# Kernel optimization log

Hardware: AMD Instinct MI355X
Metric: run time of the kernel (lower is better)

Reference implementation:

```python
import jax, jax.numpy as jnp
import numpy as np

BS = 131072
HID = 128

def _mlp(x, p):
    W1, b1, W2, b2, W3, b3 = p
    h = jnp.tanh(x @ W1 + b1)
    h = jnp.tanh(h @ W2 + b2)
    return h @ W3 + b3

def _inv2x2(M):
    # batched analytic 2x2 inverse, M: (bs,2,2)
    a, b = M[:, 0, 0], M[:, 0, 1]
    c, d = M[:, 1, 0], M[:, 1, 1]
    det = a * d - b * c
    row0 = jnp.stack([d, -b], axis=-1)
    row1 = jnp.stack([-c, a], axis=-1)
    return jnp.stack([row0, row1], axis=1) / det[:, None, None]

def _forward(y, hp, mp, gp):
    q3 = y[:, :3]           # (bs,3): x, cos q, sin q
    xq_dot = y[:, 3:5]      # (bs,2): x_dot, q_dot
    u = y[:, 5:6]           # (bs,1)
    cos_q = q3[:, 1:2]
    sin_q = q3[:, 2:3]

    def m_net(q):
        A = _mlp(q, mp).reshape(-1, 2, 2)
        return jnp.einsum('bij,bkj->bik', A, A) + jnp.eye(2, dtype=q.dtype)

    M_q_inv = m_net(q3)                                   # (bs,2,2) inverse mass matrix
    p = jnp.einsum('bij,bj->bi', _inv2x2(M_q_inv), xq_dot)  # momenta (bs,2)
    zp = jnp.concatenate([q3, p], axis=1)                 # (bs,5)

    # dH/d(x,cosq,sinq,p): samples are independent so grad of the batch-sum
    # gives per-sample gradients (matches torch.autograd.grad(H.sum(), ...)).
    dH = jax.grad(lambda z: _mlp(z, hp).sum())(zp)        # (bs,5)
    dHdx, dHdcos, dHdsin = dH[:, 0:1], dH[:, 1:2], dH[:, 2:3]
    dHdp = dH[:, 3:5]

    F = _mlp(q3, gp) * u                                  # u_dim == 1 branch
    dHdq = -sin_q * dHdcos + cos_q * dHdsin
    dx, dq = dHdp[:, 0:1], dHdp[:, 1:2]
    dp = jnp.concatenate([-dHdx, -dHdq], axis=1) + F      # (bs,2)

    # dM_inv/dt = (dM_inv/dq3) . dq3/dt  == JVP of m_net (replaces the 2x2
    # Python loop of per-element torch.autograd.grad calls).
    dq3dt = jnp.concatenate([dx, -sin_q * dq, cos_q * dq], axis=1)
    _, dM_inv_dt = jax.jvp(m_net, (q3,), (dq3dt,))        # (bs,2,2)

    ddq = jnp.einsum('bij,bj->bi', M_q_inv, dp) + jnp.einsum('bij,bj->bi', dM_inv_dt, p)
    return jnp.concatenate([dx, -sin_q * dq, cos_q * dq, ddq, jnp.zeros_like(u)], axis=1)

def setup_inputs():
    key = jax.random.key(0)
    ks = jax.random.split(key, 10)
    def w(k, fan_in, fan_out):
        return jax.random.normal(k, (fan_in, fan_out), dtype=jnp.float32) / np.float32(np.sqrt(fan_in))
    inp = {"t": 0, "y": jax.random.normal(ks[0], (BS, 6), dtype=jnp.float32)}
    dims = {"h": (5, 1), "m": (3, 4), "g": (3, 2)}
    i = 1
    for name, (din, dout) in dims.items():
        inp[name + "_W1"] = w(ks[i], din, HID)
        inp[name + "_b1"] = jnp.zeros((HID,), jnp.float32)
        inp[name + "_W2"] = w(ks[i + 1], HID, HID)
        inp[name + "_b2"] = jnp.zeros((HID,), jnp.float32)
        inp[name + "_W3"] = w(ks[i + 2], HID, dout)
        inp[name + "_b3"] = jnp.zeros((dout,), jnp.float32)
        i += 3
    return inp

def reference(t, y, h_W1, h_b1, h_W2, h_b2, h_W3, h_b3,
              m_W1, m_b1, m_W2, m_b2, m_W3, m_b3,
              g_W1, g_b1, g_W2, g_b2, g_W3, g_b3):
    hp = (h_W1, h_b1, h_W2, h_b2, h_W3, h_b3)
    mp = (m_W1, m_b1, m_W2, m_b2, m_W3, m_b3)
    gp = (g_W1, g_b1, g_W2, g_b2, g_W3, g_b3)
    return _forward(y, hp, mp, gp)
```

## Files before the change

kernel.cpp:

```cpp
#include <hip/hip_runtime.h>

#define T   32
#define LDX 132
#define NTH 512

enum { SF0 = 0, SF1, SO0, SO1, SO2, SO3, SM00, SM01, SM11, SP0, SP1,
       SV0, SV1, SV2, SDP0, SDP1, SM_N };

__device__ __forceinline__ float tanh_fast(float x) {
    float e = __expf(2.0f * x);
    return 1.0f - 2.0f / (e + 1.0f);
}

__device__ __forceinline__ float red16(float v) {
    v += __shfl_xor(v, 1);
    v += __shfl_xor(v, 2);
    v += __shfl_xor(v, 4);
    v += __shfl_xor(v, 8);
    return v;
}

template <class EPI>
__device__ __forceinline__ void mv128_fwd(const float* __restrict__ Wg,
                                          const float* in_row, int j0, EPI&& epi) {
    float acc[8];
#pragma unroll
    for (int jj = 0; jj < 8; ++jj) acc[jj] = 0.f;
    for (int i = 0; i < 128; i += 4) {
        float4 av = *(const float4*)(in_row + i);
#pragma unroll
        for (int s = 0; s < 4; ++s) {
            float a = (s == 0) ? av.x : (s == 1) ? av.y : (s == 2) ? av.z : av.w;
            const float4* wp = (const float4*)(Wg + (size_t)(i + s) * 128 + j0);
            float4 w0 = wp[0], w1 = wp[1];
            acc[0] += a * w0.x; acc[1] += a * w0.y; acc[2] += a * w0.z; acc[3] += a * w0.w;
            acc[4] += a * w1.x; acc[5] += a * w1.y; acc[6] += a * w1.z; acc[7] += a * w1.w;
        }
    }
#pragma unroll
    for (int jj = 0; jj < 8; ++jj) epi(jj, acc[jj]);
}

template <class EPI>
__device__ __forceinline__ void mv128_bwd(const float* __restrict__ Wg,
                                          const float* in_row, int j0, EPI&& epi) {
    float acc[8];
#pragma unroll
    for (int jj = 0; jj < 8; ++jj) acc[jj] = 0.f;
    for (int k = 0; k < 128; k += 4) {
        float4 tv = *(const float4*)(in_row + k);
#pragma unroll
        for (int jj = 0; jj < 8; ++jj) {
            float4 w = *(const float4*)(Wg + (size_t)(j0 + jj) * 128 + k);
            acc[jj] += tv.x * w.x + tv.y * w.y + tv.z * w.z + tv.w * w.w;
        }
    }
#pragma unroll
    for (int jj = 0; jj < 8; ++jj) epi(jj, acc[jj]);
}

template <int K, class EPI>
__device__ __forceinline__ void mvK_fwd(const float* __restrict__ Wg,
                                        const float* in, int j0, EPI&& epi) {
    float acc[8];
#pragma unroll
    for (int jj = 0; jj < 8; ++jj) acc[jj] = 0.f;
#pragma unroll
    for (int i = 0; i < K; ++i) {
        float a = in[i];
        const float4* wp = (const float4*)(Wg + (size_t)i * 128 + j0);
        float4 w0 = wp[0], w1 = wp[1];
        acc[0] += a * w0.x; acc[1] += a * w0.y; acc[2] += a * w0.z; acc[3] += a * w0.w;
        acc[4] += a * w1.x; acc[5] += a * w1.y; acc[6] += a * w1.z; acc[7] += a * w1.w;
    }
#pragma unroll
    for (int jj = 0; jj < 8; ++jj) epi(jj, acc[jj]);
}

__global__ __launch_bounds__(NTH)
void symoden_kernel(const float* __restrict__ y,
                    const float* __restrict__ hW1, const float* __restrict__ hb1,
                    const float* __restrict__ hW2, const float* __restrict__ hb2,
                    const float* __restrict__ hW3,
                    const float* __restrict__ mW1, const float* __restrict__ mb1,
                    const float* __restrict__ mW2, const float* __restrict__ mb2,
                    const float* __restrict__ mW3, const float* __restrict__ mb3,
                    const float* __restrict__ gW1, const float* __restrict__ gb1,
                    const float* __restrict__ gW2, const float* __restrict__ gb2,
                    const float* __restrict__ gW3, const float* __restrict__ gb3,
                    float* __restrict__ out) {
    __shared__ __align__(16) float Xb[T * LDX];
    __shared__ __align__(16) float Yb[T * LDX];
    __shared__ __align__(16) float Zb[T * LDX];
    __shared__ __align__(16) float Ub[T * LDX];
    __shared__ float ytile[T * 6];
    __shared__ float sm[T][SM_N];
    __shared__ float outtile[T * 6];

    const int tid = threadIdx.x;
    const int r   = tid >> 4;
    const int jg  = tid & 15;
    const int j0  = jg * 8;
    const int rowbase = blockIdx.x * T;

    if (tid < T * 6) ytile[tid] = y[(size_t)rowbase * 6 + tid];
    __syncthreads();

    const float q0 = ytile[r * 6 + 0];
    const float q1 = ytile[r * 6 + 1];
    const float q2 = ytile[r * 6 + 2];

    float* Xrow = &Xb[r * LDX];
    float* Yrow = &Yb[r * LDX];
    float* Zrow = &Zb[r * LDX];
    float* Urow = &Ub[r * LDX];

    {
        float in3[3] = {q0, q1, q2};
        mvK_fwd<3>(gW1, in3, j0, [&](int jj, float a) {
            Xrow[j0 + jj] = tanh_fast(a + gb1[j0 + jj]);
        });
    }
    __syncthreads();
    mv128_fwd(gW2, Xrow, j0, [&](int jj, float a) {
        Yrow[j0 + jj] = tanh_fast(a + gb2[j0 + jj]);
    });
    __syncthreads();
    {
        float c0 = 0.f, c1 = 0.f;
#pragma unroll
        for (int kk = 0; kk < 8; ++kk) {
            float v = Yrow[j0 + kk];
            c0 += v * gW3[(j0 + kk) * 2 + 0];
            c1 += v * gW3[(j0 + kk) * 2 + 1];
        }
        c0 = red16(c0);
        c1 = red16(c1);
        if (jg == 0) {
            float uu = ytile[r * 6 + 5];
            sm[r][SF0] = (c0 + gb3[0]) * uu;
            sm[r][SF1] = (c1 + gb3[1]) * uu;
        }
    }

    {
        float in3[3] = {q0, q1, q2};
        mvK_fwd<3>(mW1, in3, j0, [&](int jj, float a) {
            Xrow[j0 + jj] = tanh_fast(a + mb1[j0 + jj]);
        });
    }
    __syncthreads();
    mv128_fwd(mW2, Xrow, j0, [&](int jj, float a) {
        Yrow[j0 + jj] = tanh_fast(a + mb2[j0 + jj]);
    });
    __syncthreads();
    {
        float c[4] = {0.f, 0.f, 0.f, 0.f};
#pragma unroll
        for (int kk = 0; kk < 8; ++kk) {
            float v = Yrow[j0 + kk];
            const float4 w = *(const float4*)(mW3 + (size_t)(j0 + kk) * 4);
            c[0] += v * w.x; c[1] += v * w.y; c[2] += v * w.z; c[3] += v * w.w;
        }
#pragma unroll
        for (int cc = 0; cc < 4; ++cc) c[cc] = red16(c[cc]);
        if (jg == 0) {
            float o0 = c[0] + mb3[0], o1 = c[1] + mb3[1];
            float o2 = c[2] + mb3[2], o3 = c[3] + mb3[3];
            float M00 = 1.f + o0 * o0 + o1 * o1;
            float M01 = o0 * o2 + o1 * o3;
            float M11 = 1.f + o2 * o2 + o3 * o3;
            float det = M00 * M11 - M01 * M01;
            float x0 = ytile[r * 6 + 3], x1 = ytile[r * 6 + 4];
            float inv = 1.f / det;
            sm[r][SO0] = o0; sm[r][SO1] = o1; sm[r][SO2] = o2; sm[r][SO3] = o3;
            sm[r][SM00] = M00; sm[r][SM01] = M01; sm[r][SM11] = M11;
            sm[r][SP0] = (M11 * x0 - M01 * x1) * inv;
            sm[r][SP1] = (M00 * x1 - M01 * x0) * inv;
        }
#pragma unroll
        for (int kk = 0; kk < 8; ++kk) { float v = Xrow[j0 + kk]; Xrow[j0 + kk] = 1.f - v * v; }
#pragma unroll
        for (int kk = 0; kk < 8; ++kk) { float v = Yrow[j0 + kk]; Yrow[j0 + kk] = 1.f - v * v; }
    }
    __syncthreads();

    {
        float in5[5] = {q0, q1, q2, sm[r][SP0], sm[r][SP1]};
        mvK_fwd<5>(hW1, in5, j0, [&](int jj, float a) {
            Zrow[j0 + jj] = tanh_fast(a + hb1[j0 + jj]);
        });
    }
    __syncthreads();
    mv128_fwd(hW2, Zrow, j0, [&](int jj, float a) {
        float h = tanh_fast(a + hb2[j0 + jj]);
        Urow[j0 + jj] = (1.f - h * h) * hW3[j0 + jj];
    });
    __syncthreads();
    mv128_bwd(hW2, Urow, j0, [&](int jj, float a) {
        float z = Zrow[j0 + jj];
        Zrow[j0 + jj] = (1.f - z * z) * a;
    });
    {
        float d[5] = {0.f, 0.f, 0.f, 0.f, 0.f};
#pragma unroll
        for (int kk = 0; kk < 8; ++kk) {
            float s = Zrow[j0 + kk];
#pragma unroll
            for (int i = 0; i < 5; ++i) d[i] += s * hW1[(size_t)i * 128 + j0 + kk];
        }
#pragma unroll
        for (int i = 0; i < 5; ++i) d[i] = red16(d[i]);
        if (jg == 0) {
            float F0 = sm[r][SF0], F1 = sm[r][SF1];
            float dHdq = -q2 * d[1] + q1 * d[2];
            sm[r][SDP0] = -d[0] + F0;
            sm[r][SDP1] = -dHdq + F1;
            sm[r][SV0] = d[3];
            sm[r][SV1] = -q2 * d[4];
            sm[r][SV2] = q1 * d[4];
        }
    }
    __syncthreads();

    {
        float in3[3] = {sm[r][SV0], sm[r][SV1], sm[r][SV2]};
        mvK_fwd<3>(mW1, in3, j0, [&](int jj, float a) {
            Zrow[j0 + jj] = a * Xrow[j0 + jj];
        });
    }
    __syncthreads();
    mv128_fwd(mW2, Zrow, j0, [&](int jj, float a) {
        Urow[j0 + jj] = a * Yrow[j0 + jj];
    });
    {
        float c[4] = {0.f, 0.f, 0.f, 0.f};
#pragma unroll
        for (int kk = 0; kk < 8; ++kk) {
            float v = Urow[j0 + kk];
            const float4 w = *(const float4*)(mW3 + (size_t)(j0 + kk) * 4);
            c[0] += v * w.x; c[1] += v * w.y; c[2] += v * w.z; c[3] += v * w.w;
        }
#pragma unroll
        for (int cc = 0; cc < 4; ++cc) c[cc] = red16(c[cc]);
        if (jg == 0) {
            float o0 = sm[r][SO0], o1 = sm[r][SO1], o2 = sm[r][SO2], o3 = sm[r][SO3];
            float do0 = c[0], do1 = c[1], do2 = c[2], do3 = c[3];
            float dM00 = 2.f * (do0 * o0 + do1 * o1);
            float dM11 = 2.f * (do2 * o2 + do3 * o3);
            float dM01 = do0 * o2 + do1 * o3 + o0 * do2 + o1 * do3;
            float M00 = sm[r][SM00], M01 = sm[r][SM01], M11 = sm[r][SM11];
            float p0 = sm[r][SP0], p1 = sm[r][SP1];
            float dp0 = sm[r][SDP0], dp1 = sm[r][SDP1];
            float ddq0 = M00 * dp0 + M01 * dp1 + dM00 * p0 + dM01 * p1;
            float ddq1 = M01 * dp0 + M11 * dp1 + dM01 * p0 + dM11 * p1;
            outtile[r * 6 + 0] = sm[r][SV0];
            outtile[r * 6 + 1] = sm[r][SV1];
            outtile[r * 6 + 2] = sm[r][SV2];
            outtile[r * 6 + 3] = ddq0;
            outtile[r * 6 + 4] = ddq1;
            outtile[r * 6 + 5] = 0.f;
        }
    }
    __syncthreads();
    if (tid < T * 6) out[(size_t)rowbase * 6 + tid] = outtile[tid];
}

extern "C" void kernel_launch(void* const* d_in, const int* in_sizes, int n_in,
                              void* d_out, int out_size, void* d_ws, size_t ws_size,
                              hipStream_t stream) {
    (void)n_in; (void)d_ws; (void)ws_size; (void)out_size;
    const float* y   = (const float*)d_in[1];
    const float* hW1 = (const float*)d_in[2];
    const float* hb1 = (const float*)d_in[3];
    const float* hW2 = (const float*)d_in[4];
    const float* hb2 = (const float*)d_in[5];
    const float* hW3 = (const float*)d_in[6];
    const float* mW1 = (const float*)d_in[8];
    const float* mb1 = (const float*)d_in[9];
    const float* mW2 = (const float*)d_in[10];
    const float* mb2 = (const float*)d_in[11];
    const float* mW3 = (const float*)d_in[12];
    const float* mb3 = (const float*)d_in[13];
    const float* gW1 = (const float*)d_in[14];
    const float* gb1 = (const float*)d_in[15];
    const float* gW2 = (const float*)d_in[16];
    const float* gb2 = (const float*)d_in[17];
    const float* gW3 = (const float*)d_in[18];
    const float* gb3 = (const float*)d_in[19];
    float* out = (float*)d_out;

    int nrows = in_sizes[1] / 6;
    dim3 grid(nrows / T), block(NTH);
    symoden_kernel<<<grid, block, 0, stream>>>(y, hW1, hb1, hW2, hb2, hW3,
                                               mW1, mb1, mW2, mb2, mW3, mb3,
                                               gW1, gb1, gW2, gb2, gW3, gb3, out);
}
```

Before: 1.891 ms.

## Widen per-thread tile to 16 columns and keep tanh derivatives in registers

Halves the block to 256 threads, with each thread computing 16 output columns per row instead of 8. The wider tile reuses each activation load across more weights and shortens the shuffle reductions to 8 lanes. Tanh derivative factors for the first layers are kept in registers rather than rewritten to shared memory, which cuts shared-memory buffers from four to three. The cost is more registers per thread (launch bounds ask for 3 blocks per CU) and fewer threads per block, which risks spills or lower occupancy.

```diff
diff --git a/kernel.cpp b/kernel.cpp
--- a/kernel.cpp
+++ b/kernel.cpp
@@ -1,269 +1,336 @@
 #include <hip/hip_runtime.h>
 
-#define T   32
-#define LDX 132
-#define NTH 512
+#define NTH  256
+#define ROWS 32
+#define F32LD 132
 
 enum { SF0 = 0, SF1, SO0, SO1, SO2, SO3, SM00, SM01, SM11, SP0, SP1,
-       SV0, SV1, SV2, SDP0, SDP1, SM_N };
+       SDP0, SDP1, SV0, SV1, SV2, SM_N };
 
 __device__ __forceinline__ float tanh_fast(float x) {
     float e = __expf(2.0f * x);
     return 1.0f - 2.0f / (e + 1.0f);
 }
-
-__device__ __forceinline__ float red16(float v) {
+__device__ __forceinline__ float red8(float v) {
     v += __shfl_xor(v, 1);
     v += __shfl_xor(v, 2);
     v += __shfl_xor(v, 4);
-    v += __shfl_xor(v, 8);
     return v;
 }
 
-template <class EPI>
-__device__ __forceinline__ void mv128_fwd(const float* __restrict__ Wg,
-                                          const float* in_row, int j0, EPI&& epi) {
-    float acc[8];
-#pragma unroll
-    for (int jj = 0; jj < 8; ++jj) acc[jj] = 0.f;
-    for (int i = 0; i < 128; i += 4) {
-        float4 av = *(const float4*)(in_row + i);
+__device__ __forceinline__ void mv_fwd(const float* __restrict__ W, const float* Arow,
+                                       int vj0, float acc[16]) {
+#pragma unroll
+    for (int j = 0; j < 16; ++j) acc[j] = 0.f;
+    for (int k = 0; k < 128; k += 4) {
+        float4 a4 = *(const float4*)(Arow + k);
 #pragma unroll
         for (int s = 0; s < 4; ++s) {
-            float a = (s == 0) ? av.x : (s == 1) ? av.y : (s == 2) ? av.z : av.w;
-            const float4* wp = (const float4*)(Wg + (size_t)(i + s) * 128 + j0);
-            float4 w0 = wp[0], w1 = wp[1];
-            acc[0] += a * w0.x; acc[1] += a * w0.y; acc[2] += a * w0.z; acc[3] += a * w0.w;
-            acc[4] += a * w1.x; acc[5] += a * w1.y; acc[6] += a * w1.z; acc[7] += a * w1.w;
-        }
-    }
-#pragma unroll
-    for (int jj = 0; jj < 8; ++jj) epi(jj, acc[jj]);
-}
-
-template <class EPI>
-__device__ __forceinline__ void mv128_bwd(const float* __restrict__ Wg,
-                                          const float* in_row, int j0, EPI&& epi) {
-    float acc[8];
-#pragma unroll
-    for (int jj = 0; jj < 8; ++jj) acc[jj] = 0.f;
+            float a = (s == 0) ? a4.x : (s == 1) ? a4.y : (s == 2) ? a4.z : a4.w;
+            const float4* wp = (const float4*)(W + (size_t)(k + s) * 128 + vj0);
+            float4 w0 = wp[0], w1 = wp[1], w2 = wp[2], w3 = wp[3];
+            acc[0]  += a * w0.x; acc[1]  += a * w0.y; acc[2]  += a * w0.z; acc[3]  += a * w0.w;
+            acc[4]  += a * w1.x; acc[5]  += a * w1.y; acc[6]  += a * w1.z; acc[7]  += a * w1.w;
+            acc[8]  += a * w2.x; acc[9]  += a * w2.y; acc[10] += a * w2.z; acc[11] += a * w2.w;
+            acc[12] += a * w3.x; acc[13] += a * w3.y; acc[14] += a * w3.z; acc[15] += a * w3.w;
+        }
+    }
+}
+
+__device__ __forceinline__ void mv_bwd(const float* __restrict__ W, const float* Trow,
+                                       int vj0, float acc[16]) {
+#pragma unroll
+    for (int j = 0; j < 16; ++j) acc[j] = 0.f;
     for (int k = 0; k < 128; k += 4) {
-        float4 tv = *(const float4*)(in_row + k);
-#pragma unroll
-        for (int jj = 0; jj < 8; ++jj) {
-            float4 w = *(const float4*)(Wg + (size_t)(j0 + jj) * 128 + k);
-            acc[jj] += tv.x * w.x + tv.y * w.y + tv.z * w.z + tv.w * w.w;
-        }
-    }
-#pragma unroll
-    for (int jj = 0; jj < 8; ++jj) epi(jj, acc[jj]);
-}
-
-template <int K, class EPI>
-__device__ __forceinline__ void mvK_fwd(const float* __restrict__ Wg,
-                                        const float* in, int j0, EPI&& epi) {
-    float acc[8];
-#pragma unroll
-    for (int jj = 0; jj < 8; ++jj) acc[jj] = 0.f;
-#pragma unroll
-    for (int i = 0; i < K; ++i) {
-        float a = in[i];
-        const float4* wp = (const float4*)(Wg + (size_t)i * 128 + j0);
-        float4 w0 = wp[0], w1 = wp[1];
-        acc[0] += a * w0.x; acc[1] += a * w0.y; acc[2] += a * w0.z; acc[3] += a * w0.w;
-        acc[4] += a * w1.x; acc[5] += a * w1.y; acc[6] += a * w1.z; acc[7] += a * w1.w;
-    }
-#pragma unroll
-    for (int jj = 0; jj < 8; ++jj) epi(jj, acc[jj]);
-}
-
-__global__ __launch_bounds__(NTH)
-void symoden_kernel(const float* __restrict__ y,
-                    const float* __restrict__ hW1, const float* __restrict__ hb1,
-                    const float* __restrict__ hW2, const float* __restrict__ hb2,
-                    const float* __restrict__ hW3,
-                    const float* __restrict__ mW1, const float* __restrict__ mb1,
-                    const float* __restrict__ mW2, const float* __restrict__ mb2,
-                    const float* __restrict__ mW3, const float* __restrict__ mb3,
-                    const float* __restrict__ gW1, const float* __restrict__ gb1,
-                    const float* __restrict__ gW2, const float* __restrict__ gb2,
-                    const float* __restrict__ gW3, const float* __restrict__ gb3,
-                    float* __restrict__ out) {
-    __shared__ __align__(16) float Xb[T * LDX];
-    __shared__ __align__(16) float Yb[T * LDX];
-    __shared__ __align__(16) float Zb[T * LDX];
-    __shared__ __align__(16) float Ub[T * LDX];
-    __shared__ float ytile[T * 6];
-    __shared__ float sm[T][SM_N];
-    __shared__ float outtile[T * 6];
+        float4 t4 = *(const float4*)(Trow + k);
+#pragma unroll
+        for (int c = 0; c < 16; ++c) {
+            float4 w = *(const float4*)(W + (size_t)(vj0 + c) * 128 + k);
+            acc[c] += t4.x * w.x + t4.y * w.y + t4.z * w.z + t4.w * w.w;
+        }
+    }
+}
+
+__global__ __launch_bounds__(NTH, 3)
+void symoden_valu(const float* __restrict__ y,
+                  const float* __restrict__ hW1, const float* __restrict__ hb1,
+                  const float* __restrict__ hW2, const float* __restrict__ hb2,
+                  const float* __restrict__ hW3,
+                  const float* __restrict__ mW1, const float* __restrict__ mb1,
+                  const float* __restrict__ mW2, const float* __restrict__ mb2,
+                  const float* __restrict__ mW3, const float* __restrict__ mb3,
+                  const float* __restrict__ gW1, const float* __restrict__ gb1,
+                  const float* __restrict__ gW2, const float* __restrict__ gb2,
+                  const float* __restrict__ gW3, const float* __restrict__ gb3,
+                  float* __restrict__ out) {
+    __shared__ __align__(16) float A0[ROWS * F32LD];
+    __shared__ __align__(16) float A1[ROWS * F32LD];
+    __shared__ __align__(16) float FA[ROWS * F32LD];
+    __shared__ float iobuf[ROWS * 6];
+    __shared__ float sm[ROWS][SM_N];
 
     const int tid = threadIdx.x;
-    const int r   = tid >> 4;
-    const int jg  = tid & 15;
-    const int j0  = jg * 8;
-    const int rowbase = blockIdx.x * T;
-
-    if (tid < T * 6) ytile[tid] = y[(size_t)rowbase * 6 + tid];
-    __syncthreads();
-
-    const float q0 = ytile[r * 6 + 0];
-    const float q1 = ytile[r * 6 + 1];
-    const float q2 = ytile[r * 6 + 2];
-
-    float* Xrow = &Xb[r * LDX];
-    float* Yrow = &Yb[r * LDX];
-    float* Zrow = &Zb[r * LDX];
-    float* Urow = &Ub[r * LDX];
-
-    {
-        float in3[3] = {q0, q1, q2};
-        mvK_fwd<3>(gW1, in3, j0, [&](int jj, float a) {
-            Xrow[j0 + jj] = tanh_fast(a + gb1[j0 + jj]);
-        });
-    }
-    __syncthreads();
-    mv128_fwd(gW2, Xrow, j0, [&](int jj, float a) {
-        Yrow[j0 + jj] = tanh_fast(a + gb2[j0 + jj]);
-    });
-    __syncthreads();
+    const int vr  = tid >> 3;
+    const int vj0 = (tid & 7) * 16;
+    const size_t rowbase = (size_t)blockIdx.x * ROWS;
+
+    if (tid < ROWS * 6) iobuf[tid] = y[rowbase * 6 + tid];
+    __syncthreads();
+
+    const float q0 = iobuf[vr * 6 + 0];
+    const float q1 = iobuf[vr * 6 + 1];
+    const float q2 = iobuf[vr * 6 + 2];
+    float* Arow0 = &A0[vr * F32LD];
+    float* Arow1 = &A1[vr * F32LD];
+    float* FArow = &FA[vr * F32LD];
+
+    float c1f[16];
+    float c2f[16];
+    float ch1f[16];
+
+#pragma unroll
+    for (int c4 = 0; c4 < 16; c4 += 4) {
+        int col = vj0 + c4;
+        float4 w0 = *(const float4*)(gW1 + col);
+        float4 w1 = *(const float4*)(gW1 + 128 + col);
+        float4 w2 = *(const float4*)(gW1 + 256 + col);
+        float4 bb = *(const float4*)(gb1 + col);
+        float4 o;
+        o.x = tanh_fast(bb.x + q0 * w0.x + q1 * w1.x + q2 * w2.x);
+        o.y = tanh_fast(bb.y + q0 * w0.y + q1 * w1.y + q2 * w2.y);
+        o.z = tanh_fast(bb.z + q0 * w0.z + q1 * w1.z + q2 * w2.z);
+        o.w = tanh_fast(bb.w + q0 * w0.w + q1 * w1.w + q2 * w2.w);
+        *(float4*)&A0[vr * F32LD + col] = o;
+    }
+    __syncthreads();
+
+    {
+        float acc[16];
+        mv_fwd(gW2, Arow0, vj0, acc);
+#pragma unroll
+        for (int c = 0; c < 16; ++c)
+            FArow[vj0 + c] = tanh_fast(acc[c] + gb2[vj0 + c]);
+    }
+    __syncthreads();
+
     {
         float c0 = 0.f, c1 = 0.f;
 #pragma unroll
-        for (int kk = 0; kk < 8; ++kk) {
-            float v = Yrow[j0 + kk];
-            c0 += v * gW3[(j0 + kk) * 2 + 0];
-            c1 += v * gW3[(j0 + kk) * 2 + 1];
-        }
-        c0 = red16(c0);
-        c1 = red16(c1);
-        if (jg == 0) {
-            float uu = ytile[r * 6 + 5];
-            sm[r][SF0] = (c0 + gb3[0]) * uu;
-            sm[r][SF1] = (c1 + gb3[1]) * uu;
-        }
-    }
-
-    {
-        float in3[3] = {q0, q1, q2};
-        mvK_fwd<3>(mW1, in3, j0, [&](int jj, float a) {
-            Xrow[j0 + jj] = tanh_fast(a + mb1[j0 + jj]);
-        });
-    }
-    __syncthreads();
-    mv128_fwd(mW2, Xrow, j0, [&](int jj, float a) {
-        Yrow[j0 + jj] = tanh_fast(a + mb2[j0 + jj]);
-    });
-    __syncthreads();
+        for (int c4 = 0; c4 < 16; c4 += 4) {
+            float4 hv = *(const float4*)&FArow[vj0 + c4];
+#pragma unroll
+            for (int jj = 0; jj < 4; ++jj) {
+                int col = vj0 + c4 + jj;
+                float v = (jj == 0) ? hv.x : (jj == 1) ? hv.y : (jj == 2) ? hv.z : hv.w;
+                float2 w = *(const float2*)(gW3 + col * 2);
+                c0 += v * w.x;
+                c1 += v * w.y;
+            }
+        }
+        c0 = red8(c0);
+        c1 = red8(c1);
+        if ((tid & 7) == 0) {
+            float uu = iobuf[vr * 6 + 5];
+            sm[vr][SF0] = (c0 + gb3[0]) * uu;
+            sm[vr][SF1] = (c1 + gb3[1]) * uu;
+        }
+#pragma unroll
+        for (int c4 = 0; c4 < 16; c4 += 4) {
+            int col = vj0 + c4;
+            float4 w0 = *(const float4*)(mW1 + col);
+            float4 w1 = *(const float4*)(mW1 + 128 + col);
+            float4 w2 = *(const float4*)(mW1 + 256 + col);
+            float4 bb = *(const float4*)(mb1 + col);
+            float t0 = tanh_fast(bb.x + q0 * w0.x + q1 * w1.x + q2 * w2.x);
+            float t1 = tanh_fast(bb.y + q0 * w0.y + q1 * w1.y + q2 * w2.y);
+            float t2 = tanh_fast(bb.z + q0 * w0.z + q1 * w1.z + q2 * w2.z);
+            float t3 = tanh_fast(bb.w + q0 * w0.w + q1 * w1.w + q2 * w2.w);
+            c1f[c4 + 0] = 1.f - t0 * t0;
+            c1f[c4 + 1] = 1.f - t1 * t1;
+            c1f[c4 + 2] = 1.f - t2 * t2;
+            c1f[c4 + 3] = 1.f - t3 * t3;
+            *(float4*)&A0[vr * F32LD + col] = (float4){t0, t1, t2, t3};
+        }
+    }
+    __syncthreads();
+
+    {
+        float acc[16];
+        mv_fwd(mW2, Arow0, vj0, acc);
+#pragma unroll
+        for (int c = 0; c < 16; ++c) {
+            float th = tanh_fast(acc[c] + mb2[vj0 + c]);
+            FArow[vj0 + c] = th;
+            c2f[c] = 1.f - th * th;
+        }
+    }
+    __syncthreads();
+
     {
         float c[4] = {0.f, 0.f, 0.f, 0.f};
 #pragma unroll
-        for (int kk = 0; kk < 8; ++kk) {
-            float v = Yrow[j0 + kk];
-            const float4 w = *(const float4*)(mW3 + (size_t)(j0 + kk) * 4);
-            c[0] += v * w.x; c[1] += v * w.y; c[2] += v * w.z; c[3] += v * w.w;
-        }
-#pragma unroll
-        for (int cc = 0; cc < 4; ++cc) c[cc] = red16(c[cc]);
-        if (jg == 0) {
+        for (int c4 = 0; c4 < 16; c4 += 4) {
+            float4 hv = *(const float4*)&FArow[vj0 + c4];
+#pragma unroll
+            for (int jj = 0; jj < 4; ++jj) {
+                int col = vj0 + c4 + jj;
+                float v = (jj == 0) ? hv.x : (jj == 1) ? hv.y : (jj == 2) ? hv.z : hv.w;
+                float4 w = *(const float4*)(mW3 + col * 4);
+                c[0] += v * w.x; c[1] += v * w.y; c[2] += v * w.z; c[3] += v * w.w;
+            }
+        }
+#pragma unroll
+        for (int cc = 0; cc < 4; ++cc) c[cc] = red8(c[cc]);
+        if ((tid & 7) == 0) {
             float o0 = c[0] + mb3[0], o1 = c[1] + mb3[1];
             float o2 = c[2] + mb3[2], o3 = c[3] + mb3[3];
             float M00 = 1.f + o0 * o0 + o1 * o1;
             float M01 = o0 * o2 + o1 * o3;
             float M11 = 1.f + o2 * o2 + o3 * o3;
-            float det = M00 * M11 - M01 * M01;
-            float x0 = ytile[r * 6 + 3], x1 = ytile[r * 6 + 4];
-            float inv = 1.f / det;
-            sm[r][SO0] = o0; sm[r][SO1] = o1; sm[r][SO2] = o2; sm[r][SO3] = o3;
-            sm[r][SM00] = M00; sm[r][SM01] = M01; sm[r][SM11] = M11;
-            sm[r][SP0] = (M11 * x0 - M01 * x1) * inv;
-            sm[r][SP1] = (M00 * x1 - M01 * x0) * inv;
-        }
-#pragma unroll
-        for (int kk = 0; kk < 8; ++kk) { float v = Xrow[j0 + kk]; Xrow[j0 + kk] = 1.f - v * v; }
-#pragma unroll
-        for (int kk = 0; kk < 8; ++kk) { float v = Yrow[j0 + kk]; Yrow[j0 + kk] = 1.f - v * v; }
-    }
-    __syncthreads();
-
-    {
-        float in5[5] = {q0, q1, q2, sm[r][SP0], sm[r][SP1]};
-        mvK_fwd<5>(hW1, in5, j0, [&](int jj, float a) {
-            Zrow[j0 + jj] = tanh_fast(a + hb1[j0 + jj]);
-        });
-    }
-    __syncthreads();
-    mv128_fwd(hW2, Zrow, j0, [&](int jj, float a) {
-        float h = tanh_fast(a + hb2[j0 + jj]);
-        Urow[j0 + jj] = (1.f - h * h) * hW3[j0 + jj];
-    });
-    __syncthreads();
-    mv128_bwd(hW2, Urow, j0, [&](int jj, float a) {
-        float z = Zrow[j0 + jj];
-        Zrow[j0 + jj] = (1.f - z * z) * a;
-    });
-    {
-        float d[5] = {0.f, 0.f, 0.f, 0.f, 0.f};
-#pragma unroll
-        for (int kk = 0; kk < 8; ++kk) {
-            float s = Zrow[j0 + kk];
-#pragma unroll
-            for (int i = 0; i < 5; ++i) d[i] += s * hW1[(size_t)i * 128 + j0 + kk];
-        }
-#pragma unroll
-        for (int i = 0; i < 5; ++i) d[i] = red16(d[i]);
-        if (jg == 0) {
-            float F0 = sm[r][SF0], F1 = sm[r][SF1];
-            float dHdq = -q2 * d[1] + q1 * d[2];
-            sm[r][SDP0] = -d[0] + F0;
-            sm[r][SDP1] = -dHdq + F1;
-            sm[r][SV0] = d[3];
-            sm[r][SV1] = -q2 * d[4];
-            sm[r][SV2] = q1 * d[4];
-        }
-    }
-    __syncthreads();
-
-    {
-        float in3[3] = {sm[r][SV0], sm[r][SV1], sm[r][SV2]};
-        mvK_fwd<3>(mW1, in3, j0, [&](int jj, float a) {
-            Zrow[j0 + jj] = a * Xrow[j0 + jj];
-        });
-    }
-    __syncthreads();
-    mv128_fwd(mW2, Zrow, j0, [&](int jj, float a) {
-        Urow[j0 + jj] = a * Yrow[j0 + jj];
-    });
+            float inv = 1.f / (M00 * M11 - M01 * M01);
+            float x0 = iobuf[vr * 6 + 3], x1 = iobuf[vr * 6 + 4];
+            sm[vr][SO0] = o0; sm[vr][SO1] = o1; sm[vr][SO2] = o2; sm[vr][SO3] = o3;
+            sm[vr][SM00] = M00; sm[vr][SM01] = M01; sm[vr][SM11] = M11;
+            sm[vr][SP0] = (M11 * x0 - M01 * x1) * inv;
+            sm[vr][SP1] = (M00 * x1 - M01 * x0) * inv;
+        }
+    }
+    __syncthreads();
+
+    {
+        float p0 = sm[vr][SP0], p1 = sm[vr][SP1];
+#pragma unroll
+        for (int c4 = 0; c4 < 16; c4 += 4) {
+            int col = vj0 + c4;
+            float4 w0 = *(const float4*)(hW1 + col);
+            float4 w1 = *(const float4*)(hW1 + 128 + col);
+            float4 w2 = *(const float4*)(hW1 + 256 + col);
+            float4 w3 = *(const float4*)(hW1 + 384 + col);
+            float4 w4 = *(const float4*)(hW1 + 512 + col);
+            float4 bb = *(const float4*)(hb1 + col);
+            float t0 = tanh_fast(bb.x + q0 * w0.x + q1 * w1.x + q2 * w2.x + p0 * w3.x + p1 * w4.x);
+            float t1 = tanh_fast(bb.y + q0 * w0.y + q1 * w1.y + q2 * w2.y + p0 * w3.y + p1 * w4.y);
+            float t2 = tanh_fast(bb.z + q0 * w0.z + q1 * w1.z + q2 * w2.z + p0 * w3.z + p1 * w4.z);
+            float t3 = tanh_fast(bb.w + q0 * w0.w + q1 * w1.w + q2 * w2.w + p0 * w3.w + p1 * w4.w);
+            ch1f[c4 + 0] = 1.f - t0 * t0;
+            ch1f[c4 + 1] = 1.f - t1 * t1;
+            ch1f[c4 + 2] = 1.f - t2 * t2;
+            ch1f[c4 + 3] = 1.f - t3 * t3;
+            *(float4*)&A0[vr * F32LD + col] = (float4){t0, t1, t2, t3};
+        }
+    }
+    __syncthreads();
+
+    {
+        float acc[16];
+        mv_fwd(hW2, Arow0, vj0, acc);
+#pragma unroll
+        for (int c = 0; c < 16; ++c) {
+            float th = tanh_fast(acc[c] + hb2[vj0 + c]);
+            Arow1[vj0 + c] = (1.f - th * th) * hW3[vj0 + c];
+        }
+    }
+    __syncthreads();
+
+    {
+        float acc[16];
+        mv_bwd(hW2, Arow1, vj0, acc);
+#pragma unroll
+        for (int c = 0; c < 16; ++c)
+            FArow[vj0 + c] = acc[c];
+    }
+    __syncthreads();
+
+    {
+        float d0 = 0.f, d1 = 0.f, d2 = 0.f, d3 = 0.f, d4 = 0.f;
+#pragma unroll
+        for (int c4 = 0; c4 < 16; c4 += 4) {
+            float4 rv = *(const float4*)&FArow[vj0 + c4];
+#pragma unroll
+            for (int jj = 0; jj < 4; ++jj) {
+                int col = vj0 + c4 + jj;
+                float r = (jj == 0) ? rv.x : (jj == 1) ? rv.y : (jj == 2) ? rv.z : rv.w;
+                float s = r * ch1f[c4 + jj];
+                d0 += s * hW1[col];
+                d1 += s * hW1[128 + col];
+                d2 += s * hW1[256 + col];
+                d3 += s * hW1[384 + col];
+                d4 += s * hW1[512 + col];
+            }
+        }
+        d0 = red8(d0); d1 = red8(d1); d2 = red8(d2); d3 = red8(d3); d4 = red8(d4);
+        if ((tid & 7) == 0) {
+            float dHdq = -q2 * d1 + q1 * d2;
+            float v0 = d3, v1 = -q2 * d4, v2 = q1 * d4;
+            sm[vr][SDP0] = -d0 + sm[vr][SF0];
+            sm[vr][SDP1] = -dHdq + sm[vr][SF1];
+            sm[vr][SV0] = v0; sm[vr][SV1] = v1; sm[vr][SV2] = v2;
+            iobuf[vr * 6 + 0] = v0;
+            iobuf[vr * 6 + 1] = v1;
+            iobuf[vr * 6 + 2] = v2;
+        }
+    }
+    __syncthreads();
+
+    {
+        float v0 = sm[vr][SV0], v1 = sm[vr][SV1], v2 = sm[vr][SV2];
+#pragma unroll
+        for (int c4 = 0; c4 < 16; c4 += 4) {
+            int col = vj0 + c4;
+            float4 w0 = *(const float4*)(mW1 + col);
+            float4 w1 = *(const float4*)(mW1 + 128 + col);
+            float4 w2 = *(const float4*)(mW1 + 256 + col);
+            float4 o;
+            o.x = (v0 * w0.x + v1 * w1.x + v2 * w2.x) * c1f[c4 + 0];
+            o.y = (v0 * w0.y + v1 * w1.y + v2 * w2.y) * c1f[c4 + 1];
+            o.z = (v0 * w0.z + v1 * w1.z + v2 * w2.z) * c1f[c4 + 2];
+            o.w = (v0 * w0.w + v1 * w1.w + v2 * w2.w) * c1f[c4 + 3];
+            *(float4*)&A1[vr * F32LD + col] = o;
+        }
+    }
+    __syncthreads();
+
+    {
+        float acc[16];
+        mv_fwd(mW2, Arow1, vj0, acc);
+#pragma unroll
+        for (int c = 0; c < 16; ++c)
+            FArow[vj0 + c] = acc[c] * c2f[c];
+    }
+    __syncthreads();
+
     {
         float c[4] = {0.f, 0.f, 0.f, 0.f};
 #pragma unroll
-        for (int kk = 0; kk < 8; ++kk) {
-            float v = Urow[j0 + kk];
-            const float4 w = *(const float4*)(mW3 + (size_t)(j0 + kk) * 4);
-            c[0] += v * w.x; c[1] += v * w.y; c[2] += v * w.z; c[3] += v * w.w;
-        }
-#pragma unroll
-        for (int cc = 0; cc < 4; ++cc) c[cc] = red16(c[cc]);
-        if (jg == 0) {
-            float o0 = sm[r][SO0], o1 = sm[r][SO1], o2 = sm[r][SO2], o3 = sm[r][SO3];
+        for (int c4 = 0; c4 < 16; c4 += 4) {
+            float4 uv = *(const float4*)&FArow[vj0 + c4];
+#pragma unroll
+            for (int jj = 0; jj < 4; ++jj) {
+                int col = vj0 + c4 + jj;
+                float u = (jj == 0) ? uv.x : (jj == 1) ? uv.y : (jj == 2) ? uv.z : uv.w;
+                float4 w = *(const float4*)(mW3 + col * 4);
+                c[0] += u * w.x; c[1] += u * w.y; c[2] += u * w.z; c[3] += u * w.w;
+            }
+        }
+#pragma unroll
+        for (int cc = 0; cc < 4; ++cc) c[cc] = red8(c[cc]);
+        if ((tid & 7) == 0) {
+            float o0 = sm[vr][SO0], o1 = sm[vr][SO1], o2 = sm[vr][SO2], o3 = sm[vr][SO3];
             float do0 = c[0], do1 = c[1], do2 = c[2], do3 = c[3];
             float dM00 = 2.f * (do0 * o0 + do1 * o1);
             float dM11 = 2.f * (do2 * o2 + do3 * o3);
             float dM01 = do0 * o2 + do1 * o3 + o0 * do2 + o1 * do3;
-            float M00 = sm[r][SM00], M01 = sm[r][SM01], M11 = sm[r][SM11];
-            float p0 = sm[r][SP0], p1 = sm[r][SP1];
-            float dp0 = sm[r][SDP0], dp1 = sm[r][SDP1];
-            float ddq0 = M00 * dp0 + M01 * dp1 + dM00 * p0 + dM01 * p1;
-            float ddq1 = M01 * dp0 + M11 * dp1 + dM01 * p0 + dM11 * p1;
-            outtile[r * 6 + 0] = sm[r][SV0];
-            outtile[r * 6 + 1] = sm[r][SV1];
-            outtile[r * 6 + 2] = sm[r][SV2];
-            outtile[r * 6 + 3] = ddq0;
-            outtile[r * 6 + 4] = ddq1;
-            outtile[r * 6 + 5] = 0.f;
-        }
-    }
-    __syncthreads();
-    if (tid < T * 6) out[(size_t)rowbase * 6 + tid] = outtile[tid];
+            float M00 = sm[vr][SM00], M01 = sm[vr][SM01], M11 = sm[vr][SM11];
+            float p0 = sm[vr][SP0], p1 = sm[vr][SP1];
+            float dp0 = sm[vr][SDP0], dp1 = sm[vr][SDP1];
+            iobuf[vr * 6 + 3] = M00 * dp0 + M01 * dp1 + dM00 * p0 + dM01 * p1;
+            iobuf[vr * 6 + 4] = M01 * dp0 + M11 * dp1 + dM01 * p0 + dM11 * p1;
+            iobuf[vr * 6 + 5] = 0.f;
+        }
+    }
+    __syncthreads();
+
+    if (tid < ROWS * 6) out[rowbase * 6 + tid] = iobuf[tid];
 }
 
 extern "C" void kernel_launch(void* const* d_in, const int* in_sizes, int n_in,
@@ -291,8 +358,8 @@
     float* out = (float*)d_out;
 
     int nrows = in_sizes[1] / 6;
-    dim3 grid(nrows / T), block(NTH);
-    symoden_kernel<<<grid, block, 0, stream>>>(y, hW1, hb1, hW2, hb2, hW3,
-                                               mW1, mb1, mW2, mb2, mW3, mb3,
-                                               gW1, gb1, gW2, gb2, gW3, gb3, out);
-}
+    dim3 grid(nrows / ROWS), block(NTH);
+    symoden_valu<<<grid, block, 0, stream>>>(y, hW1, hb1, hW2, hb2, hW3,
+                                             mW1, mb1, mW2, mb2, mW3, mb3,
+                                             gW1, gb1, gW2, gb2, gW3, gb3, out);
+}
```

After: 2.815 ms. +48.8%, slower.
